# Kernel tuning notes

Hardware: AMD Instinct MI355X
Metric: run time of the kernel (lower is better)

The kernel has to match this reference:

```python
import jax, jax.numpy as jnp
import numpy as np

EPS = 1e-6

def _rmsnorm(x, w):
    # normalize over last (head_dim) axis
    return x * jax.lax.rsqrt(jnp.mean(x * x, axis=-1, keepdims=True) + EPS) * w

def _rope(x, cos, sin):
    # x: [B, H, S, D]; cos/sin: [S, D]
    d = x.shape[-1]
    x1, x2 = x[..., : d // 2], x[..., d // 2 :]
    rot = jnp.concatenate([-x2, x1], axis=-1)
    return x * cos[None, None] + rot * sin[None, None]

def setup_inputs() -> dict:
    key = jax.random.key(0)
    B, S, D_MODEL = 1, 2048, 2048
    HEADS, HEAD_DIM, NKV = 32, 64, 8
    d_out = HEADS * HEAD_DIM
    kv_d_out = NKV * HEAD_DIM
    ks = jax.random.split(key, 8)
    x = jax.random.normal(ks[0], (B, S, D_MODEL), dtype=jnp.float32)
    # RoPE tables
    inv_freq = 1.0 / (10000.0 ** (jnp.arange(0, HEAD_DIM, 2, dtype=jnp.float32) / HEAD_DIM))
    pos = jnp.arange(S, dtype=jnp.float32)
    ang = pos[:, None] * inv_freq[None, :]            # [S, D/2]
    ang = jnp.concatenate([ang, ang], axis=-1)        # [S, D]
    sin, cos = jnp.sin(ang), jnp.cos(ang)
    mask = jnp.tril(jnp.ones((S, S), dtype=bool))     # causal: True = attend
    sd = 0.02
    Wq = jax.random.normal(ks[1], (D_MODEL, d_out), dtype=jnp.float32) * sd
    Wk = jax.random.normal(ks[2], (D_MODEL, kv_d_out), dtype=jnp.float32) * sd
    Wv = jax.random.normal(ks[3], (D_MODEL, kv_d_out), dtype=jnp.float32) * sd
    Wo = jax.random.normal(ks[4], (d_out, D_MODEL), dtype=jnp.float32) * sd
    bo = jnp.zeros((D_MODEL,), dtype=jnp.float32)
    q_scale = jnp.ones((HEAD_DIM,), dtype=jnp.float32)
    k_scale = jnp.ones((HEAD_DIM,), dtype=jnp.float32)
    return {"x": x, "sin": sin, "cos": cos, "mask": mask, "Wq": Wq, "Wk": Wk,
            "Wv": Wv, "Wo": Wo, "bo": bo, "q_scale": q_scale, "k_scale": k_scale}

def reference(x, sin, cos, mask, Wq, Wk, Wv, Wo, bo, q_scale, k_scale):
    B, S, _ = x.shape
    HEADS, HEAD_DIM, NKV = 32, 64, 8
    GS = HEADS // NKV  # group size = 4
    q = (x @ Wq).reshape(B, S, HEADS, HEAD_DIM).transpose(0, 2, 1, 3)  # [B,H,S,D]
    k = (x @ Wk).reshape(B, S, NKV, HEAD_DIM).transpose(0, 2, 1, 3)    # [B,G,S,D]
    v = (x @ Wv).reshape(B, S, NKV, HEAD_DIM).transpose(0, 2, 1, 3)    # [B,G,S,D]
    q = _rmsnorm(q, q_scale)
    k = _rmsnorm(k, k_scale)
    q = _rope(q, cos, sin)
    k = _rope(k, cos, sin)
    # GQA without materializing repeated k/v: group query heads per kv group
    qg = q.reshape(B, NKV, GS, S, HEAD_DIM)
    scale = 1.0 / jnp.sqrt(jnp.asarray(HEAD_DIM, dtype=x.dtype))
    scores = jnp.einsum('bghqd,bgkd->bghqk', qg, k) * scale  # [B,G,Gs,S,S]
    scores = jnp.where(mask[None, None, None], scores, jnp.asarray(-jnp.inf, dtype=scores.dtype))
    attn = jax.nn.softmax(scores, axis=-1)
    out = jnp.einsum('bghqk,bgkd->bghqd', attn, v)            # [B,G,Gs,S,D]
    out = out.reshape(B, HEADS, S, HEAD_DIM).transpose(0, 2, 1, 3).reshape(B, S, HEADS * HEAD_DIM)
    return out @ Wo + bo
```

## Files before the change

### kernel.cpp

```cpp
#include <hip/hip_runtime.h>
#include <stdint.h>


typedef __bf16 bf16x8 __attribute__((ext_vector_type(8)));
typedef float f32x4 __attribute__((ext_vector_type(4)));

#define MFMA_BF16(a, b, c) __builtin_amdgcn_mfma_f32_16x16x32_bf16(a, b, c, 0, 0, 0)

#if __has_builtin(__builtin_amdgcn_exp2f)
#define EXP2F(x) __builtin_amdgcn_exp2f(x)
#else
#define EXP2F(x) __expf((x) * 0.69314718055994531f)
#endif

#define QSCALE 0.18033688011112042f
#define SHIFT2 11.541560327111707f

__device__ __forceinline__ unsigned short f2bf(float f) {
  unsigned int u = __float_as_uint(f);
  u += 0x7fffu + ((u >> 16) & 1u);
  return (unsigned short)(u >> 16);
}
__device__ __forceinline__ float bf2f(unsigned short b) {
  return __uint_as_float(((unsigned int)b) << 16);
}

__device__ __forceinline__ void gload_lds16(const unsigned short* gsrc,
                                            unsigned short* ldst) {
  __builtin_amdgcn_global_load_lds(
      (const __attribute__((address_space(1))) unsigned int*)gsrc,
      (__attribute__((address_space(3))) unsigned int*)ldst, 16, 0, 0);
}

__global__ __launch_bounds__(256) void cvt_bf16(const float* __restrict__ X,
                                                unsigned short* __restrict__ Y, int n) {
  int i = (blockIdx.x * 256 + threadIdx.x) * 4;
  if (i < n) {
    float4 v = *(const float4*)&X[i];
    ushort4 o;
    o.x = f2bf(v.x); o.y = f2bf(v.y); o.z = f2bf(v.z); o.w = f2bf(v.w);
    *(ushort4*)&Y[i] = o;
  }
}

__global__ __launch_bounds__(256) void transpose_w(const float* __restrict__ W,
                                                   unsigned short* __restrict__ T,
                                                   int K, int N) {
  __shared__ float tile[64][65];
  int kb = blockIdx.y * 64, nb = blockIdx.x * 64;
  int tid = threadIdx.x;
#pragma unroll
  for (int i = 0; i < 16; i++) {
    int idx = tid + i * 256;
    int r = idx >> 6, c = idx & 63;
    tile[r][c] = W[(size_t)(kb + r) * N + nb + c];
  }
  __syncthreads();
#pragma unroll
  for (int i = 0; i < 16; i++) {
    int idx = tid + i * 256;
    int r = idx >> 6, c = idx & 63;
    T[(size_t)(nb + r) * K + kb + c] = f2bf(tile[c][r]);
  }
}

#define GEMM_CORE(A_, B_, m0_, n0_, K_)                                        \
  int quad = lane >> 4, l16 = lane & 15;                                       \
  int wrow = (w & 1) * 32, wcol = (w >> 1) * 64;                               \
  int rsub = lane >> 3, csub = lane & 7;                                       \
  int chunk = csub ^ rsub;                                                     \
  const unsigned short* gA0 = &A_[(size_t)(m0_ + w * 16 + rsub) * K_ + chunk * 8]; \
  const unsigned short* gA1 = gA0 + 8 * K_;                                    \
  const unsigned short* gB0 = &B_[(size_t)(n0_ + w * 32 + rsub) * K_ + chunk * 8]; \
  const unsigned short* gB1 = gB0 + 8 * K_;                                    \
  const unsigned short* gB2 = gB0 + 16 * K_;                                   \
  const unsigned short* gB3 = gB0 + 24 * K_;                                   \
  unsigned short* lA0 = As + (w * 16) * 64 + lane * 8;                         \
  unsigned short* lA1 = lA0 + 8 * 64;                                          \
  unsigned short* lB0 = Bs + (w * 32) * 64 + lane * 8;                         \
  unsigned short* lB1 = lB0 + 8 * 64;                                          \
  unsigned short* lB2 = lB0 + 16 * 64;                                         \
  unsigned short* lB3 = lB0 + 24 * 64;                                         \
  int slotL = quad ^ (l16 & 7);                                                \
  f32x4 acc[2][4];                                                             \
  _Pragma("unroll") for (int i = 0; i < 2; i++)                                \
      _Pragma("unroll") for (int j = 0; j < 4; j++)                            \
          acc[i][j] = (f32x4){0.f, 0.f, 0.f, 0.f};                             \
  for (int k0 = 0; k0 < K_; k0 += 64) {                                        \
    __syncthreads();                                                           \
    gload_lds16(gA0 + k0, lA0);                                                \
    gload_lds16(gA1 + k0, lA1);                                                \
    gload_lds16(gB0 + k0, lB0);                                                \
    gload_lds16(gB1 + k0, lB1);                                                \
    gload_lds16(gB2 + k0, lB2);                                                \
    gload_lds16(gB3 + k0, lB3);                                                \
    __syncthreads();                                                           \
    bf16x8 af[2][2], bfr[4][2];                                                \
    _Pragma("unroll") for (int i = 0; i < 2; i++) {                            \
      int base = (wrow + i * 16 + l16) * 64;                                   \
      af[i][0] = *(const bf16x8*)&As[base + slotL * 8];                        \
      af[i][1] = *(const bf16x8*)&As[base + (slotL ^ 4) * 8];                  \
    }                                                                          \
    _Pragma("unroll") for (int j = 0; j < 4; j++) {                            \
      int base = (wcol + j * 16 + l16) * 64;                                   \
      bfr[j][0] = *(const bf16x8*)&Bs[base + slotL * 8];                       \
      bfr[j][1] = *(const bf16x8*)&Bs[base + (slotL ^ 4) * 8];                 \
    }                                                                          \
    _Pragma("unroll") for (int kc = 0; kc < 2; kc++)                           \
        _Pragma("unroll") for (int i = 0; i < 2; i++)                          \
            _Pragma("unroll") for (int j = 0; j < 4; j++)                      \
                acc[i][j] = MFMA_BF16(af[i][kc], bfr[j][kc], acc[i][j]);       \
  }

__global__ __launch_bounds__(256, 4) void gemm_qkv(const unsigned short* __restrict__ A,
                                                   const unsigned short* __restrict__ B,
                                                   const float* __restrict__ sinp,
                                                   const float* __restrict__ cosp,
                                                   const float* __restrict__ q_scale,
                                                   const float* __restrict__ k_scale,
                                                   unsigned short* __restrict__ qh,
                                                   unsigned short* __restrict__ kh,
                                                   unsigned short* __restrict__ vtmp) {
  __shared__ __align__(16) unsigned short As[64 * 64];
  __shared__ __align__(16) unsigned short Bs[128 * 64];
  int tid = threadIdx.x;
  int w = tid >> 6, lane = tid & 63;
  int m0 = blockIdx.y * 64;
  int n0 = blockIdx.x * 128;
  GEMM_CORE(A, B, m0, n0, 2048)

  int hd = blockIdx.x * 2 + (w >> 1);
  if (hd < 40) {
    const float* scl = (hd < 32) ? q_scale : k_scale;
    float wsc[4];
#pragma unroll
    for (int j = 0; j < 4; j++) wsc[j] = scl[j * 16 + l16];
    float oscale = (hd < 32) ? QSCALE : 1.0f;
#pragma unroll
    for (int i = 0; i < 2; i++)
#pragma unroll
      for (int r = 0; r < 4; r++) {
        float ss = 0.f;
#pragma unroll
        for (int j = 0; j < 4; j++) ss += acc[i][j][r] * acc[i][j][r];
#pragma unroll
        for (int off = 8; off; off >>= 1) ss += __shfl_xor(ss, off);
        float inv = rsqrtf(ss * (1.f / 64.f) + 1e-6f);
        int s = m0 + wrow + i * 16 + quad * 4 + r;
        float xn[4];
#pragma unroll
        for (int j = 0; j < 4; j++) xn[j] = acc[i][j][r] * inv * wsc[j];
#pragma unroll
        for (int j = 0; j < 4; j++) {
          int d = j * 16 + l16;
          float rot = (j < 2) ? -xn[j + 2] : xn[j - 2];
          float out = (xn[j] * cosp[s * 64 + d] + rot * sinp[s * 64 + d]) * oscale;
          if (hd < 32) qh[(size_t)s * 2048 + hd * 64 + d] = f2bf(out);
          else         kh[(size_t)s * 512 + (hd - 32) * 64 + d] = f2bf(out);
        }
      }
  } else {
    int g = hd - 40;
#pragma unroll
    for (int i = 0; i < 2; i++)
#pragma unroll
      for (int r = 0; r < 4; r++) {
        int s = m0 + wrow + i * 16 + quad * 4 + r;
#pragma unroll
        for (int j = 0; j < 4; j++)
          vtmp[(size_t)s * 512 + g * 64 + j * 16 + l16] = f2bf(acc[i][j][r]);
      }
  }
}

__global__ __launch_bounds__(256, 4) void gemm_out(const unsigned short* __restrict__ A,
                                                   const unsigned short* __restrict__ B,
                                                   float* __restrict__ C,
                                                   const float* __restrict__ bias) {
  __shared__ __align__(16) unsigned short As[64 * 64];
  __shared__ __align__(16) unsigned short Bs[128 * 64];
  int tid = threadIdx.x;
  int w = tid >> 6, lane = tid & 63;
  int m0 = blockIdx.y * 64;
  int n0 = blockIdx.x * 128;
  GEMM_CORE(A, B, m0, n0, 2048)

#pragma unroll
  for (int i = 0; i < 2; i++) {
    int row = m0 + wrow + i * 16 + quad * 4;
#pragma unroll
    for (int j = 0; j < 4; j++) {
      int col = n0 + wcol + j * 16 + l16;
      float b = bias[col];
#pragma unroll
      for (int r = 0; r < 4; r++)
        C[(size_t)(row + r) * 2048 + col] = acc[i][j][r] + b;
    }
  }
}

__global__ __launch_bounds__(256) void v_transpose(const unsigned short* __restrict__ vtmp,
                                                   unsigned short* __restrict__ vt) {
  __shared__ unsigned short tile[64][65];
  int s0 = blockIdx.x * 64;
  int g = blockIdx.y;
  int tid = threadIdx.x;
#pragma unroll
  for (int i = 0; i < 16; i++) {
    int idx = tid + i * 256;
    int r = idx >> 6, c = idx & 63;
    tile[r][c] = vtmp[(size_t)(s0 + r) * 512 + g * 64 + c];
  }
  __syncthreads();
#pragma unroll
  for (int i = 0; i < 16; i++) {
    int idx = tid + i * 256;
    int d = idx >> 6, sl = idx & 63;
    vt[(size_t)(g * 64 + d) * 2048 + s0 + sl] = tile[sl][d];
  }
}

__global__ __launch_bounds__(256, 4) void attention(const unsigned short* __restrict__ qh,
                                                    const unsigned short* __restrict__ kh,
                                                    const unsigned short* __restrict__ vt,
                                                    unsigned short* __restrict__ Opart,
                                                    float* __restrict__ Lpart) {
  int h = blockIdx.y;
  int g = h >> 2;
  int z = blockIdx.z;
  int tile = (blockIdx.x + blockIdx.y) & 31;
  int q0 = tile * 64;
  int w = threadIdx.x >> 6;
  int lane = threadIdx.x & 63;
  int quad = lane >> 4;
  int l16 = lane & 15;
  int qrow0 = q0 + w * 16;

  __shared__ __align__(16) unsigned short Ks[64 * 64];
  __shared__ __align__(16) unsigned short Vs[64 * 64];
  __shared__ __align__(16) unsigned short Plds[4][16 * 72];
  unsigned short* P = &Plds[w][0];

  int rsub = lane >> 3;
  int csub = lane & 7;
  int chunk = csub ^ rsub;

  const unsigned short* kg0 = &kh[(size_t)(w * 16 + rsub) * 512 + g * 64 + chunk * 8];
  const unsigned short* kg1 = kg0 + 8 * 512;
  const unsigned short* vg0 = &vt[(size_t)(g * 64 + w * 16 + rsub) * 2048 + chunk * 8];
  const unsigned short* vg1 = vg0 + 8 * 2048;
  unsigned short* kl0 = &Ks[(w * 16) * 64] + lane * 8;
  unsigned short* kl1 = kl0 + 8 * 64;
  unsigned short* vl0 = &Vs[(w * 16) * 64] + lane * 8;
  unsigned short* vl1 = vl0 + 8 * 64;

  int posL = quad ^ (l16 & 7);
  int fL = l16 * 64 + posL * 8;
  int fH = l16 * 64 + (posL ^ 4) * 8;

  bf16x8 aq0 = *(const bf16x8*)&qh[(size_t)(qrow0 + l16) * 2048 + h * 64 + quad * 8];
  bf16x8 aq1 = *(const bf16x8*)&qh[(size_t)(qrow0 + l16) * 2048 + h * 64 + 32 + quad * 8];

  f32x4 o[4];
#pragma unroll
  for (int j = 0; j < 4; j++) o[j] = (f32x4){0.f, 0.f, 0.f, 0.f};
  float l_run[4] = {0.f, 0.f, 0.f, 0.f};

  int T = tile + 1;
  int it0 = z ? (T >> 1) : 0;
  int it1 = z ? T : (T >> 1);
  for (int it = it0; it < it1; ++it) {
    int n0 = it << 6;
    __syncthreads();
    gload_lds16(kg0 + (size_t)n0 * 512, kl0);
    gload_lds16(kg1 + (size_t)n0 * 512, kl1);
    gload_lds16(vg0 + n0, vl0);
    gload_lds16(vg1 + n0, vl1);
    __syncthreads();

    f32x4 s[4];
#pragma unroll
    for (int t = 0; t < 4; ++t) {
      bf16x8 kfl = *(const bf16x8*)&Ks[t * 1024 + fL];
      bf16x8 kfh = *(const bf16x8*)&Ks[t * 1024 + fH];
      f32x4 zz = (f32x4){0.f, 0.f, 0.f, 0.f};
      zz = MFMA_BF16(aq0, kfl, zz);
      s[t] = MFMA_BF16(aq1, kfh, zz);
    }

    if (it == T - 1) {
#pragma unroll
      for (int t = 0; t < 4; ++t) {
        int key = n0 + t * 16 + l16;
#pragma unroll
        for (int r = 0; r < 4; ++r) {
          int row = qrow0 + quad * 4 + r;
          float p = (key <= row) ? EXP2F(s[t][r] - SHIFT2) : 0.f;
          l_run[r] += p;
          P[(quad * 4 + r) * 72 + t * 16 + l16] = f2bf(p);
        }
      }
    } else {
#pragma unroll
      for (int t = 0; t < 4; ++t)
#pragma unroll
        for (int r = 0; r < 4; ++r) {
          float p = EXP2F(s[t][r] - SHIFT2);
          l_run[r] += p;
          P[(quad * 4 + r) * 72 + t * 16 + l16] = f2bf(p);
        }
    }
    __threadfence_block();
    bf16x8 pf0 = *(const bf16x8*)&P[l16 * 72 + quad * 8];
    bf16x8 pf1 = *(const bf16x8*)&P[l16 * 72 + 32 + quad * 8];

#pragma unroll
    for (int j = 0; j < 4; ++j) {
      bf16x8 vfl = *(const bf16x8*)&Vs[j * 1024 + fL];
      bf16x8 vfh = *(const bf16x8*)&Vs[j * 1024 + fH];
      o[j] = MFMA_BF16(pf0, vfl, o[j]);
      o[j] = MFMA_BF16(pf1, vfh, o[j]);
    }
  }

#pragma unroll
  for (int r = 0; r < 4; r++) {
    float sum = l_run[r];
#pragma unroll
    for (int off = 8; off; off >>= 1) sum += __shfl_xor(sum, off);
    if (l16 == 0)
      Lpart[(size_t)z * 65536 + (qrow0 + quad * 4 + r) * 32 + h] = sum;
  }
#pragma unroll
  for (int j = 0; j < 4; j++)
#pragma unroll
    for (int r = 0; r < 4; r++)
      Opart[((size_t)z * 2048 + qrow0 + quad * 4 + r) * 2048 + h * 64 + j * 16 + l16] =
          f2bf(o[j][r]);
}

__global__ __launch_bounds__(256) void combine(const unsigned short* __restrict__ Opart,
                                               const float* __restrict__ Lpart,
                                               unsigned short* __restrict__ aout) {
  int idx = blockIdx.x * 256 + threadIdx.x;
  int s = idx >> 9;
  int col = (idx & 511) * 4;
  int h = col >> 6;
  float l = Lpart[s * 32 + h] + Lpart[65536 + s * 32 + h];
  float linv = 1.f / l;
  ushort4 a = *(const ushort4*)&Opart[(size_t)s * 2048 + col];
  ushort4 b = *(const ushort4*)&Opart[(size_t)(2048 + s) * 2048 + col];
  ushort4 o;
  o.x = f2bf((bf2f(a.x) + bf2f(b.x)) * linv);
  o.y = f2bf((bf2f(a.y) + bf2f(b.y)) * linv);
  o.z = f2bf((bf2f(a.z) + bf2f(b.z)) * linv);
  o.w = f2bf((bf2f(a.w) + bf2f(b.w)) * linv);
  *(ushort4*)&aout[(size_t)s * 2048 + col] = o;
}

extern "C" void kernel_launch(void* const* d_in, const int* in_sizes, int n_in,
                              void* d_out, int out_size, void* d_ws, size_t ws_size,
                              hipStream_t stream) {
  (void)in_sizes; (void)n_in; (void)out_size; (void)ws_size;
  const float* x    = (const float*)d_in[0];
  const float* sinp = (const float*)d_in[1];
  const float* cosp = (const float*)d_in[2];
  const float* Wq = (const float*)d_in[4];
  const float* Wk = (const float*)d_in[5];
  const float* Wv = (const float*)d_in[6];
  const float* Wo = (const float*)d_in[7];
  const float* bo = (const float*)d_in[8];
  const float* q_scale = (const float*)d_in[9];
  const float* k_scale = (const float*)d_in[10];
  float* outp = (float*)d_out;

  uint8_t* ws = (uint8_t*)d_ws;
  const size_t MB = 1024 * 1024;
  unsigned short* xb    = (unsigned short*)(ws);
  unsigned short* Wqkvt = (unsigned short*)(ws + 8 * MB);
  unsigned short* Wot   = (unsigned short*)(ws + 20 * MB);
  unsigned short* qh    = (unsigned short*)(ws + 28 * MB);
  unsigned short* kh    = (unsigned short*)(ws + 36 * MB);
  unsigned short* vtmp  = (unsigned short*)(ws + 38 * MB);
  unsigned short* vt    = (unsigned short*)(ws + 40 * MB);
  unsigned short* aout  = (unsigned short*)(ws + 42 * MB);
  unsigned short* Opart = (unsigned short*)(ws + 50 * MB);
  float*          Lpart = (float*)(ws + 66 * MB);

  cvt_bf16<<<4096, 256, 0, stream>>>(x, xb, 2048 * 2048);
  transpose_w<<<dim3(32, 32), 256, 0, stream>>>(Wq, Wqkvt, 2048, 2048);
  transpose_w<<<dim3(8, 32), 256, 0, stream>>>(Wk, Wqkvt + 2048 * 2048, 2048, 512);
  transpose_w<<<dim3(8, 32), 256, 0, stream>>>(Wv, Wqkvt + 2560 * 2048, 2048, 512);
  transpose_w<<<dim3(32, 32), 256, 0, stream>>>(Wo, Wot, 2048, 2048);
  gemm_qkv<<<dim3(24, 32), 256, 0, stream>>>(xb, Wqkvt, sinp, cosp, q_scale, k_scale,
                                             qh, kh, vtmp);
  v_transpose<<<dim3(32, 8), 256, 0, stream>>>(vtmp, vt);
  attention<<<dim3(32, 32, 2), 256, 0, stream>>>(qh, kh, vt, Opart, Lpart);
  combine<<<4096, 256, 0, stream>>>(Opart, Lpart, aout);
  gemm_out<<<dim3(16, 32), 256, 0, stream>>>(aout, Wot, outp, bo);
}
```

Measured before the change: 239.6 us.

## Merge weight transposes, use 2-wave GEMM tiles, pack P stores in attention

Merges the four weight-transpose launches into one kernel and widens its stores to ushort2. Both GEMMs move from 4 waves with 32x64 tiles to 2 waves with 64x64 tiles, so each wave issues more MFMAs per LDS load. In attention, P is written as packed bf16x4 vectors, and v_transpose permutes the key order to match. The aims are fewer launches, more register-level reuse in the GEMMs, and fewer LDS store instructions, at the cost of fewer waves per block and higher register pressure.

```diff
diff --git a/kernel.cpp b/kernel.cpp
--- a/kernel.cpp
+++ b/kernel.cpp
@@ -3,6 +3,7 @@
 
 
 typedef __bf16 bf16x8 __attribute__((ext_vector_type(8)));
+typedef __bf16 bf16x4v __attribute__((ext_vector_type(4)));
 typedef float f32x4 __attribute__((ext_vector_type(4)));
 
 #define MFMA_BF16(a, b, c) __builtin_amdgcn_mfma_f32_16x16x32_bf16(a, b, c, 0, 0, 0)
@@ -43,12 +44,23 @@
   }
 }
 
-__global__ __launch_bounds__(256) void transpose_w(const float* __restrict__ W,
-                                                   unsigned short* __restrict__ T,
-                                                   int K, int N) {
+__global__ __launch_bounds__(256) void transpose_all(const float* __restrict__ Wq,
+                                                     const float* __restrict__ Wk,
+                                                     const float* __restrict__ Wv,
+                                                     const float* __restrict__ Wo,
+                                                     unsigned short* __restrict__ Wqkvt,
+                                                     unsigned short* __restrict__ Wot) {
+  int bx = blockIdx.x;
+  const float* W;
+  unsigned short* T;
+  int N, nb;
+  if (bx < 32)      { W = Wq; T = Wqkvt;                     N = 2048; nb = bx * 64; }
+  else if (bx < 40) { W = Wk; T = Wqkvt + 2048 * 2048;       N = 512;  nb = (bx - 32) * 64; }
+  else if (bx < 48) { W = Wv; T = Wqkvt + (size_t)2560 * 2048; N = 512; nb = (bx - 40) * 64; }
+  else              { W = Wo; T = Wot;                       N = 2048; nb = (bx - 48) * 64; }
+  int kb = blockIdx.y * 64;
+  int tid = threadIdx.x;
   __shared__ float tile[64][65];
-  int kb = blockIdx.y * 64, nb = blockIdx.x * 64;
-  int tid = threadIdx.x;
 #pragma unroll
   for (int i = 0; i < 16; i++) {
     int idx = tid + i * 256;
@@ -57,62 +69,54 @@
   }
   __syncthreads();
 #pragma unroll
-  for (int i = 0; i < 16; i++) {
+  for (int i = 0; i < 8; i++) {
     int idx = tid + i * 256;
-    int r = idx >> 6, c = idx & 63;
-    T[(size_t)(nb + r) * K + kb + c] = f2bf(tile[c][r]);
-  }
-}
-
-#define GEMM_CORE(A_, B_, m0_, n0_, K_)                                        \
+    int r = idx >> 5, cp = idx & 31;
+    ushort2 o;
+    o.x = f2bf(tile[2 * cp][r]);
+    o.y = f2bf(tile[2 * cp + 1][r]);
+    *(ushort2*)&T[(size_t)(nb + r) * 2048 + kb + 2 * cp] = o;
+  }
+}
+
+#define GEMM_CORE2(A_, B_, m0_, n0_, K_)                                       \
   int quad = lane >> 4, l16 = lane & 15;                                       \
-  int wrow = (w & 1) * 32, wcol = (w >> 1) * 64;                               \
   int rsub = lane >> 3, csub = lane & 7;                                       \
   int chunk = csub ^ rsub;                                                     \
-  const unsigned short* gA0 = &A_[(size_t)(m0_ + w * 16 + rsub) * K_ + chunk * 8]; \
-  const unsigned short* gA1 = gA0 + 8 * K_;                                    \
-  const unsigned short* gB0 = &B_[(size_t)(n0_ + w * 32 + rsub) * K_ + chunk * 8]; \
-  const unsigned short* gB1 = gB0 + 8 * K_;                                    \
-  const unsigned short* gB2 = gB0 + 16 * K_;                                   \
-  const unsigned short* gB3 = gB0 + 24 * K_;                                   \
-  unsigned short* lA0 = As + (w * 16) * 64 + lane * 8;                         \
-  unsigned short* lA1 = lA0 + 8 * 64;                                          \
-  unsigned short* lB0 = Bs + (w * 32) * 64 + lane * 8;                         \
-  unsigned short* lB1 = lB0 + 8 * 64;                                          \
-  unsigned short* lB2 = lB0 + 16 * 64;                                         \
-  unsigned short* lB3 = lB0 + 24 * 64;                                         \
+  const unsigned short* gA = &A_[(size_t)(m0_ + w * 32 + rsub) * K_ + chunk * 8]; \
+  const unsigned short* gB = &B_[(size_t)(n0_ + w * 64 + rsub) * K_ + chunk * 8]; \
+  unsigned short* lA = As + (w * 32) * 64 + lane * 8;                          \
+  unsigned short* lB = Bs + (w * 64) * 64 + lane * 8;                          \
   int slotL = quad ^ (l16 & 7);                                                \
-  f32x4 acc[2][4];                                                             \
-  _Pragma("unroll") for (int i = 0; i < 2; i++)                                \
+  f32x4 acc[4][4];                                                             \
+  _Pragma("unroll") for (int i = 0; i < 4; i++)                                \
       _Pragma("unroll") for (int j = 0; j < 4; j++)                            \
           acc[i][j] = (f32x4){0.f, 0.f, 0.f, 0.f};                             \
   for (int k0 = 0; k0 < K_; k0 += 64) {                                        \
     __syncthreads();                                                           \
-    gload_lds16(gA0 + k0, lA0);                                                \
-    gload_lds16(gA1 + k0, lA1);                                                \
-    gload_lds16(gB0 + k0, lB0);                                                \
-    gload_lds16(gB1 + k0, lB1);                                                \
-    gload_lds16(gB2 + k0, lB2);                                                \
-    gload_lds16(gB3 + k0, lB3);                                                \
+    _Pragma("unroll") for (int c = 0; c < 4; c++)                              \
+        gload_lds16(gA + (size_t)c * 8 * K_ + k0, lA + c * 8 * 64);            \
+    _Pragma("unroll") for (int c = 0; c < 8; c++)                              \
+        gload_lds16(gB + (size_t)c * 8 * K_ + k0, lB + c * 8 * 64);            \
     __syncthreads();                                                           \
-    bf16x8 af[2][2], bfr[4][2];                                                \
-    _Pragma("unroll") for (int i = 0; i < 2; i++) {                            \
-      int base = (wrow + i * 16 + l16) * 64;                                   \
+    bf16x8 af[4][2], bfr[4][2];                                                \
+    _Pragma("unroll") for (int i = 0; i < 4; i++) {                            \
+      int base = (i * 16 + l16) * 64;                                          \
       af[i][0] = *(const bf16x8*)&As[base + slotL * 8];                        \
       af[i][1] = *(const bf16x8*)&As[base + (slotL ^ 4) * 8];                  \
     }                                                                          \
     _Pragma("unroll") for (int j = 0; j < 4; j++) {                            \
-      int base = (wcol + j * 16 + l16) * 64;                                   \
+      int base = (w * 64 + j * 16 + l16) * 64;                                 \
       bfr[j][0] = *(const bf16x8*)&Bs[base + slotL * 8];                       \
       bfr[j][1] = *(const bf16x8*)&Bs[base + (slotL ^ 4) * 8];                 \
     }                                                                          \
     _Pragma("unroll") for (int kc = 0; kc < 2; kc++)                           \
-        _Pragma("unroll") for (int i = 0; i < 2; i++)                          \
+        _Pragma("unroll") for (int i = 0; i < 4; i++)                          \
             _Pragma("unroll") for (int j = 0; j < 4; j++)                      \
                 acc[i][j] = MFMA_BF16(af[i][kc], bfr[j][kc], acc[i][j]);       \
   }
 
-__global__ __launch_bounds__(256, 4) void gemm_qkv(const unsigned short* __restrict__ A,
+__global__ __launch_bounds__(128, 3) void gemm_qkv(const unsigned short* __restrict__ A,
                                                    const unsigned short* __restrict__ B,
                                                    const float* __restrict__ sinp,
                                                    const float* __restrict__ cosp,
@@ -127,9 +131,9 @@
   int w = tid >> 6, lane = tid & 63;
   int m0 = blockIdx.y * 64;
   int n0 = blockIdx.x * 128;
-  GEMM_CORE(A, B, m0, n0, 2048)
-
-  int hd = blockIdx.x * 2 + (w >> 1);
+  GEMM_CORE2(A, B, m0, n0, 2048)
+
+  int hd = blockIdx.x * 2 + w;
   if (hd < 40) {
     const float* scl = (hd < 32) ? q_scale : k_scale;
     float wsc[4];
@@ -137,7 +141,7 @@
     for (int j = 0; j < 4; j++) wsc[j] = scl[j * 16 + l16];
     float oscale = (hd < 32) ? QSCALE : 1.0f;
 #pragma unroll
-    for (int i = 0; i < 2; i++)
+    for (int i = 0; i < 4; i++)
 #pragma unroll
       for (int r = 0; r < 4; r++) {
         float ss = 0.f;
@@ -146,7 +150,7 @@
 #pragma unroll
         for (int off = 8; off; off >>= 1) ss += __shfl_xor(ss, off);
         float inv = rsqrtf(ss * (1.f / 64.f) + 1e-6f);
-        int s = m0 + wrow + i * 16 + quad * 4 + r;
+        int s = m0 + i * 16 + quad * 4 + r;
         float xn[4];
 #pragma unroll
         for (int j = 0; j < 4; j++) xn[j] = acc[i][j][r] * inv * wsc[j];
@@ -162,10 +166,10 @@
   } else {
     int g = hd - 40;
 #pragma unroll
-    for (int i = 0; i < 2; i++)
+    for (int i = 0; i < 4; i++)
 #pragma unroll
       for (int r = 0; r < 4; r++) {
-        int s = m0 + wrow + i * 16 + quad * 4 + r;
+        int s = m0 + i * 16 + quad * 4 + r;
 #pragma unroll
         for (int j = 0; j < 4; j++)
           vtmp[(size_t)s * 512 + g * 64 + j * 16 + l16] = f2bf(acc[i][j][r]);
@@ -173,7 +177,7 @@
   }
 }
 
-__global__ __launch_bounds__(256, 4) void gemm_out(const unsigned short* __restrict__ A,
+__global__ __launch_bounds__(128, 3) void gemm_out(const unsigned short* __restrict__ A,
                                                    const unsigned short* __restrict__ B,
                                                    float* __restrict__ C,
                                                    const float* __restrict__ bias) {
@@ -183,14 +187,14 @@
   int w = tid >> 6, lane = tid & 63;
   int m0 = blockIdx.y * 64;
   int n0 = blockIdx.x * 128;
-  GEMM_CORE(A, B, m0, n0, 2048)
-
-#pragma unroll
-  for (int i = 0; i < 2; i++) {
-    int row = m0 + wrow + i * 16 + quad * 4;
+  GEMM_CORE2(A, B, m0, n0, 2048)
+
+#pragma unroll
+  for (int i = 0; i < 4; i++) {
+    int row = m0 + i * 16 + quad * 4;
 #pragma unroll
     for (int j = 0; j < 4; j++) {
-      int col = n0 + wcol + j * 16 + l16;
+      int col = n0 + w * 64 + j * 16 + l16;
       float b = bias[col];
 #pragma unroll
       for (int r = 0; r < 4; r++)
@@ -215,8 +219,9 @@
 #pragma unroll
   for (int i = 0; i < 16; i++) {
     int idx = tid + i * 256;
-    int d = idx >> 6, sl = idx & 63;
-    vt[(size_t)(g * 64 + d) * 2048 + s0 + sl] = tile[sl][d];
+    int d = idx >> 6, slot = idx & 63;
+    int key = (slot & 3) * 16 + (slot >> 2);
+    vt[(size_t)(g * 64 + d) * 2048 + s0 + slot] = tile[key][d];
   }
 }
 
@@ -288,6 +293,7 @@
       s[t] = MFMA_BF16(aq1, kfh, zz);
     }
 
+    float pv[4][4];
     if (it == T - 1) {
 #pragma unroll
       for (int t = 0; t < 4; ++t) {
@@ -297,7 +303,7 @@
           int row = qrow0 + quad * 4 + r;
           float p = (key <= row) ? EXP2F(s[t][r] - SHIFT2) : 0.f;
           l_run[r] += p;
-          P[(quad * 4 + r) * 72 + t * 16 + l16] = f2bf(p);
+          pv[t][r] = p;
         }
       }
     } else {
@@ -307,8 +313,15 @@
         for (int r = 0; r < 4; ++r) {
           float p = EXP2F(s[t][r] - SHIFT2);
           l_run[r] += p;
-          P[(quad * 4 + r) * 72 + t * 16 + l16] = f2bf(p);
+          pv[t][r] = p;
         }
+    }
+#pragma unroll
+    for (int r = 0; r < 4; ++r) {
+      bf16x4v pk;
+      pk[0] = (__bf16)pv[0][r]; pk[1] = (__bf16)pv[1][r];
+      pk[2] = (__bf16)pv[2][r]; pk[3] = (__bf16)pv[3][r];
+      *(bf16x4v*)&P[(quad * 4 + r) * 72 + l16 * 4] = pk;
     }
     __threadfence_block();
     bf16x8 pf0 = *(const bf16x8*)&P[l16 * 72 + quad * 8];
@@ -388,14 +401,11 @@
   float*          Lpart = (float*)(ws + 66 * MB);
 
   cvt_bf16<<<4096, 256, 0, stream>>>(x, xb, 2048 * 2048);
-  transpose_w<<<dim3(32, 32), 256, 0, stream>>>(Wq, Wqkvt, 2048, 2048);
-  transpose_w<<<dim3(8, 32), 256, 0, stream>>>(Wk, Wqkvt + 2048 * 2048, 2048, 512);
-  transpose_w<<<dim3(8, 32), 256, 0, stream>>>(Wv, Wqkvt + 2560 * 2048, 2048, 512);
-  transpose_w<<<dim3(32, 32), 256, 0, stream>>>(Wo, Wot, 2048, 2048);
-  gemm_qkv<<<dim3(24, 32), 256, 0, stream>>>(xb, Wqkvt, sinp, cosp, q_scale, k_scale,
+  transpose_all<<<dim3(80, 32), 256, 0, stream>>>(Wq, Wk, Wv, Wo, Wqkvt, Wot);
+  gemm_qkv<<<dim3(24, 32), 128, 0, stream>>>(xb, Wqkvt, sinp, cosp, q_scale, k_scale,
                                              qh, kh, vtmp);
   v_transpose<<<dim3(32, 8), 256, 0, stream>>>(vtmp, vt);
   attention<<<dim3(32, 32, 2), 256, 0, stream>>>(qh, kh, vt, Opart, Lpart);
   combine<<<4096, 256, 0, stream>>>(Opart, Lpart, aout);
-  gemm_out<<<dim3(16, 32), 256, 0, stream>>>(aout, Wot, outp, bo);
-}
+  gemm_out<<<dim3(16, 32), 128, 0, stream>>>(aout, Wot, outp, bo);
+}
```

After: 238.7 us. About the same (-0.4%).
